# Kernel tuning notes

Measured on AMD Instinct MI355X. Metric: run time of the kernel, lower is better.

The kernel has to match this reference:

```python
import jax, jax.numpy as jnp
import numpy as np

HEADS = 16
DIM = 1024


def setup_inputs() -> dict:
    key = jax.random.key(0)
    ks = jax.random.split(key, 9)
    B, N, D = 2, 2048, DIM
    s = 1.0 / np.sqrt(D)
    x = jax.random.normal(ks[0], (B, N, D), dtype=jnp.float32)
    Wq = jax.random.normal(ks[1], (D, D), dtype=jnp.float32) * s
    Wk = jax.random.normal(ks[2], (D, D), dtype=jnp.float32) * s
    Wv = jax.random.normal(ks[3], (D, D), dtype=jnp.float32) * s
    Wo = jax.random.normal(ks[4], (D, D), dtype=jnp.float32) * s
    bq = jax.random.normal(ks[5], (D,), dtype=jnp.float32) * 0.01
    bk = jax.random.normal(ks[6], (D,), dtype=jnp.float32) * 0.01
    bv = jax.random.normal(ks[7], (D,), dtype=jnp.float32) * 0.01
    bo = jax.random.normal(ks[8], (D,), dtype=jnp.float32) * 0.01
    return {"x": x, "Wq": Wq, "bq": bq, "Wk": Wk, "bk": bk,
            "Wv": Wv, "bv": bv, "Wo": Wo, "bo": bo}


def reference(x, Wq, bq, Wk, bk, Wv, bv, Wo, bo):
    B, N, D = x.shape
    H = HEADS
    hd = D // H
    scale = hd ** (-0.5)
    # projections; split heads -> [B, H, N, hd]
    q = (x @ Wq + bq).reshape(B, N, H, hd).transpose(0, 2, 1, 3)
    k = (x @ Wk + bk).reshape(B, N, H, hd).transpose(0, 2, 1, 3)
    v = (x @ Wv + bv).reshape(B, N, H, hd).transpose(0, 2, 1, 3)
    # full [B, H, N, N] scores (faithful to naive torch implementation)
    attn = jnp.einsum('bhqd,bhkd->bhqk', q, k) * scale
    attn = jax.nn.softmax(attn, axis=-1)
    # dropout is identity in eval mode
    out = jnp.einsum('bhqk,bhkd->bhqd', attn, v)
    out = out.transpose(0, 2, 1, 3).reshape(B, N, D)
    return out @ Wo + bo
```

## Files before the change

kernel.cpp:

```cpp
#include <hip/hip_runtime.h>

#define HEADS 16
#define HD 64
#define SEQ 2048
#define DMODEL 1024
#define BATCH 2
#define MTOT (BATCH*SEQ)
#define KVB 64
#define NKH 16

typedef unsigned short u16;
typedef __bf16 bf16;
typedef bf16 bf16x8 __attribute__((ext_vector_type(8)));
typedef float f32x4 __attribute__((ext_vector_type(4)));
typedef float f32x16 __attribute__((ext_vector_type(16)));
typedef unsigned short u16x8 __attribute__((ext_vector_type(8)));
typedef unsigned short u16x4 __attribute__((ext_vector_type(4)));

static __device__ __forceinline__ u16 f2bf(float f) {
  bf16 b = (bf16)f;
  return __builtin_bit_cast(u16, b);
}

static __device__ __forceinline__ void async16(u16* lds_base, const u16* g) {
  __builtin_amdgcn_global_load_lds(
      (const __attribute__((address_space(1))) unsigned int*)g,
      (__attribute__((address_space(3))) unsigned int*)lds_base,
      16, 0, 0);
}

__global__ __launch_bounds__(256) void k_cvt(const float* __restrict__ in,
                                             u16* __restrict__ out, int n8) {
  int i = blockIdx.x * blockDim.x + threadIdx.x;
  if (i >= n8) return;
  const float4* p = (const float4*)(in + (size_t)i * 8);
  float4 a = p[0], b = p[1];
  u16x8 r;
  r[0] = f2bf(a.x); r[1] = f2bf(a.y); r[2] = f2bf(a.z); r[3] = f2bf(a.w);
  r[4] = f2bf(b.x); r[5] = f2bf(b.y); r[6] = f2bf(b.z); r[7] = f2bf(b.w);
  *(u16x8*)(out + (size_t)i * 8) = r;
}

__global__ __launch_bounds__(256) void k_cvtT(const float* __restrict__ W0, const float* __restrict__ W1,
                                              const float* __restrict__ W2, const float* __restrict__ W3,
                                              u16* __restrict__ T0, u16* __restrict__ T1,
                                              u16* __restrict__ T2, u16* __restrict__ T3) {
  const float* W = blockIdx.z == 0 ? W0 : blockIdx.z == 1 ? W1 : blockIdx.z == 2 ? W2 : W3;
  u16*         T = blockIdx.z == 0 ? T0 : blockIdx.z == 1 ? T1 : blockIdx.z == 2 ? T2 : T3;
  __shared__ u16 tile[64 * 68];
  int t = threadIdx.x;
  int kb = blockIdx.y * 64, nb = blockIdx.x * 64;
#pragma unroll
  for (int i = 0; i < 4; ++i) {
    int c = t * 4 + i;
    int row = c >> 4;
    int c4 = c & 15;
    float4 v = *(const float4*)&W[(size_t)(kb + row) * DMODEL + nb + c4 * 4];
    tile[row * 68 + c4 * 4 + 0] = f2bf(v.x);
    tile[row * 68 + c4 * 4 + 1] = f2bf(v.y);
    tile[row * 68 + c4 * 4 + 2] = f2bf(v.z);
    tile[row * 68 + c4 * 4 + 3] = f2bf(v.w);
  }
  __syncthreads();
#pragma unroll
  for (int i = 0; i < 2; ++i) {
    int c = t * 2 + i;
    int n = c >> 3;
    int k8 = c & 7;
    u16x8 v;
#pragma unroll
    for (int e = 0; e < 8; ++e) v[e] = tile[(k8 * 8 + e) * 68 + n];
    *(u16x8*)&T[(size_t)(nb + n) * DMODEL + kb + k8 * 8] = v;
  }
}

template <int MODE>
__global__ __launch_bounds__(256) void k_gemm(
    const u16* __restrict__ A,
    const u16* __restrict__ BT0, const u16* __restrict__ BT1, const u16* __restrict__ BT2,
    const float* __restrict__ b0, const float* __restrict__ b1, const float* __restrict__ b2,
    void* __restrict__ O0, void* __restrict__ O1, void* __restrict__ O2,
    int M, int N, int K) {
  const u16* BT = blockIdx.z == 0 ? BT0 : blockIdx.z == 1 ? BT1 : BT2;
  const float* bias = blockIdx.z == 0 ? b0 : blockIdx.z == 1 ? b1 : b2;
  void* Out = blockIdx.z == 0 ? O0 : blockIdx.z == 1 ? O1 : O2;

  __shared__ u16 Ads[128 * 32];
  __shared__ u16 Bds[128 * 32];
  int tid = threadIdx.x, wid = tid >> 6, lane = tid & 63;
  int r = lane & 15, g = lane >> 4;
  int wm = wid >> 1, wn = wid & 1;
  int m0 = blockIdx.y * 128, n0 = blockIdx.x * 128;

  f32x4 acc[4][4];
  f32x4 zero4 = {0.f, 0.f, 0.f, 0.f};
#pragma unroll
  for (int mt = 0; mt < 4; ++mt)
#pragma unroll
    for (int nt = 0; nt < 4; ++nt) acc[mt][nt] = zero4;

  int srow = lane >> 2;
  int scb = lane & 3;

  for (int k0 = 0; k0 < K; k0 += 32) {
#pragma unroll
    for (int tt = 0; tt < 2; ++tt) {
      int inst = wid * 2 + tt;
      int row = inst * 16 + srow;
      async16(&Ads[inst * 512], &A[(size_t)(m0 + row) * K + k0 + scb * 8]);
      async16(&Bds[inst * 512], &BT[(size_t)(n0 + row) * K + k0 + scb * 8]);
    }
    __syncthreads();
    bf16x8 af[4], bfv[4];
#pragma unroll
    for (int mt = 0; mt < 4; ++mt)
      af[mt] = *(const bf16x8*)&Ads[(wm * 64 + mt * 16 + r) * 32 + g * 8];
#pragma unroll
    for (int nt = 0; nt < 4; ++nt)
      bfv[nt] = *(const bf16x8*)&Bds[(wn * 64 + nt * 16 + r) * 32 + g * 8];
#pragma unroll
    for (int mt = 0; mt < 4; ++mt)
#pragma unroll
      for (int nt = 0; nt < 4; ++nt)
        acc[mt][nt] = __builtin_amdgcn_mfma_f32_16x16x32_bf16(af[mt], bfv[nt], acc[mt][nt], 0, 0, 0);
    __syncthreads();
  }

  const float qs = 0.18033688011112042f;
#pragma unroll
  for (int nt = 0; nt < 4; ++nt) {
    int col = n0 + wn * 64 + nt * 16 + r;
    float bv = bias[col];
#pragma unroll
    for (int mt = 0; mt < 4; ++mt) {
      int rowb = m0 + wm * 64 + mt * 16 + g * 4;
      if (MODE == 0) {
        int b = rowb >> 11;
        int h = col >> 6, d = col & (HD - 1);
        if (blockIdx.z == 2) {
          int n = rowb & (SEQ - 1);
          int np = (n & ~12) | ((n & 4) << 1) | ((n & 8) >> 1);
          u16x4 pk;
#pragma unroll
          for (int j = 0; j < 4; ++j) pk[j] = f2bf(acc[mt][nt][j] + bv);
          *(u16x4*)&((u16*)Out)[((size_t)((b * HEADS + h) * HD + d)) * SEQ + np] = pk;
        } else {
          float sc = (blockIdx.z == 0) ? qs : 1.0f;
#pragma unroll
          for (int j = 0; j < 4; ++j) {
            int row = rowb + j;
            int n = row & (SEQ - 1);
            ((u16*)Out)[((size_t)(b * HEADS + h) * SEQ + n) * HD + d] = f2bf((acc[mt][nt][j] + bv) * sc);
          }
        }
      } else {
#pragma unroll
        for (int j = 0; j < 4; ++j)
          ((float*)Out)[(size_t)(rowb + j) * N + col] = acc[mt][nt][j] + bv;
      }
    }
  }
}

__global__ __launch_bounds__(512, 4) void k_attn(const u16* __restrict__ Q,
                                                 const u16* __restrict__ Kg,
                                                 const u16* __restrict__ Vt,
                                                 u16* __restrict__ Oa) {
  __shared__ u16 lds[2][2][2][KVB * 64];

  int tid = threadIdx.x, wid = tid >> 6, lane = tid & 63;
  int l31 = lane & 31, hi = lane >> 5;
  int h = wid >> 2, s = wid & 3;

  int fid = blockIdx.y * gridDim.x + blockIdx.x;
  int swz = (fid & 7) * 64 + (fid >> 3);
  int qt = swz & 15;
  int bh = swz >> 4;

  const size_t kbase = (size_t)bh * SEQ * HD;
  const size_t vbase = (size_t)bh * HD * SEQ;
  int q0 = qt * 128 + s * 32;

  bf16x8 qf[4];
#pragma unroll
  for (int db = 0; db < 4; ++db)
    qf[db] = *(const bf16x8*)&Q[kbase + (size_t)(q0 + l31) * HD + db * 16 + hi * 8];

  int swz7 = l31 & 7;
  int coff[4];
#pragma unroll
  for (int i = 0; i < 4; ++i) coff[i] = ((2 * i + hi) ^ swz7) * 8;

  f32x16 zero16 = {0.f,0.f,0.f,0.f,0.f,0.f,0.f,0.f,0.f,0.f,0.f,0.f,0.f,0.f,0.f,0.f};
  f32x16 oacc0 = zero16, oacc1 = zero16, lacc = zero16;

  u16x8 onesb;
#pragma unroll
  for (int e = 0; e < 8; ++e) onesb[e] = 0x3F80;
  bf16x8 ones = __builtin_bit_cast(bf16x8, onesb);

  auto STAGE = [&](int b, int kc) {
    int kof = (h * NKH + kc) * KVB;
#pragma unroll
    for (int i = 0; i < 2; ++i) {
      int inst = s * 2 + i;
      int rr = inst * 8 + (lane >> 3);
      int ch = (lane & 7) ^ (rr & 7);
      async16(&lds[b][h][0][inst * 512], &Kg[kbase + (size_t)(kof + rr) * HD + ch * 8]);
      async16(&lds[b][h][1][inst * 512], &Vt[vbase + (size_t)rr * SEQ + kof + ch * 8]);
    }
  };

  auto BODY = [&](int buf, int kc) {
    if (kc + 1 < NKH) STAGE(buf ^ 1, kc + 1);

    const u16* Kb = &lds[buf][h][0][0];
    const u16* Vb = &lds[buf][h][1][0];

    f32x16 s0 = zero16, s1 = zero16;
#pragma unroll
    for (int db = 0; db < 4; ++db) {
      bf16x8 kf0 = *(const bf16x8*)&Kb[l31 * 64 + coff[db]];
      bf16x8 kf1 = *(const bf16x8*)&Kb[2048 + l31 * 64 + coff[db]];
      s0 = __builtin_amdgcn_mfma_f32_32x32x16_bf16(kf0, qf[db], s0, 0, 0, 0);
      s1 = __builtin_amdgcn_mfma_f32_32x32x16_bf16(kf1, qf[db], s1, 0, 0, 0);
    }

#pragma unroll
    for (int t = 0; t < 4; ++t) {
      u16x8 pk8;
#pragma unroll
      for (int e = 0; e < 8; ++e) {
        float sv = (t & 2) ? ((t & 1) ? s1[8 + e] : s1[e])
                           : ((t & 1) ? s0[8 + e] : s0[e]);
        pk8[e] = f2bf(__builtin_amdgcn_exp2f(sv));
      }
      bf16x8 pa = __builtin_bit_cast(bf16x8, pk8);

      lacc = __builtin_amdgcn_mfma_f32_32x32x16_bf16(pa, ones, lacc, 0, 0, 0);
      bf16x8 vf0 = *(const bf16x8*)&Vb[l31 * 64 + coff[t]];
      bf16x8 vf1 = *(const bf16x8*)&Vb[2048 + l31 * 64 + coff[t]];
      oacc0 = __builtin_amdgcn_mfma_f32_32x32x16_bf16(pa, vf0, oacc0, 0, 0, 0);
      oacc1 = __builtin_amdgcn_mfma_f32_32x32x16_bf16(pa, vf1, oacc1, 0, 0, 0);
    }

    asm volatile("s_waitcnt vmcnt(0)" ::: "memory");
    __builtin_amdgcn_sched_barrier(0);
    __builtin_amdgcn_s_barrier();
    __builtin_amdgcn_sched_barrier(0);
  };

  STAGE(0, 0);
  asm volatile("s_waitcnt vmcnt(0)" ::: "memory");
  __builtin_amdgcn_sched_barrier(0);
  __builtin_amdgcn_s_barrier();
  __builtin_amdgcn_sched_barrier(0);

  for (int kc = 0; kc < NKH; kc += 2) {
    BODY(0, kc);
    BODY(1, kc + 1);
  }

  float* cf = (float*)&lds[0][0][0][0];
  if (h == 1) {
#pragma unroll
    for (int r = 0; r < 16; ++r) {
      cf[s * 3072 + r * 64 + lane] = oacc0[r];
      cf[s * 3072 + 1024 + r * 64 + lane] = oacc1[r];
      cf[s * 3072 + 2048 + r * 64 + lane] = lacc[r];
    }
  }
  __syncthreads();
  if (h == 0) {
#pragma unroll
    for (int r = 0; r < 16; ++r) {
      oacc0[r] += cf[s * 3072 + r * 64 + lane];
      oacc1[r] += cf[s * 3072 + 1024 + r * 64 + lane];
      lacc[r]  += cf[s * 3072 + 2048 + r * 64 + lane];
    }
    int b = bh >> 4, hh = bh & 15;
#pragma unroll
    for (int reg = 0; reg < 16; ++reg) {
      int q = q0 + (reg & 3) + 8 * (reg >> 2) + 4 * hi;
      float inv = 1.0f / lacc[reg];
      size_t rowoff = ((size_t)(b * SEQ + q)) * DMODEL + hh * HD;
      Oa[rowoff + l31]      = f2bf(oacc0[reg] * inv);
      Oa[rowoff + 32 + l31] = f2bf(oacc1[reg] * inv);
    }
  }
}

extern "C" void kernel_launch(void* const* d_in, const int* in_sizes, int n_in,
                              void* d_out, int out_size, void* d_ws, size_t ws_size,
                              hipStream_t stream) {
  const float* x  = (const float*)d_in[0];
  const float* Wq = (const float*)d_in[1];
  const float* bq = (const float*)d_in[2];
  const float* Wk = (const float*)d_in[3];
  const float* bk = (const float*)d_in[4];
  const float* Wv = (const float*)d_in[5];
  const float* bv = (const float*)d_in[6];
  const float* Wo = (const float*)d_in[7];
  const float* bo = (const float*)d_in[8];

  char* ws = (char*)d_ws;
  const size_t MB = 1024 * 1024;
  u16* xb    = (u16*)(ws);
  u16* wqT   = (u16*)(ws + 8 * MB);
  u16* wkT   = (u16*)(ws + 10 * MB);
  u16* wvT   = (u16*)(ws + 12 * MB);
  u16* woT   = (u16*)(ws + 14 * MB);
  u16* qbuf  = (u16*)(ws + 16 * MB);
  u16* kbuf  = (u16*)(ws + 24 * MB);
  u16* vbufT = (u16*)(ws + 32 * MB);
  u16* abuf  = (u16*)(ws + 40 * MB);

  k_cvt<<<2048, 256, 0, stream>>>(x, xb, (MTOT * DMODEL) / 8);
  k_cvtT<<<dim3(16, 16, 4), 256, 0, stream>>>(Wq, Wk, Wv, Wo, wqT, wkT, wvT, woT);
  k_gemm<0><<<dim3(DMODEL / 128, MTOT / 128, 3), 256, 0, stream>>>(
      xb, wqT, wkT, wvT, bq, bk, bv, qbuf, kbuf, vbufT, MTOT, DMODEL, DMODEL);
  k_attn<<<dim3(SEQ / 128, BATCH * HEADS), 512, 0, stream>>>(qbuf, kbuf, vbufT, abuf);
  k_gemm<1><<<dim3(DMODEL / 128, MTOT / 128, 1), 256, 0, stream>>>(
      abuf, woT, woT, woT, bo, bo, bo, d_out, d_out, d_out, MTOT, DMODEL, DMODEL);
}
```

Measured before the change: 119.7 us.

## Double-buffer GEMM LDS tiles and raise wave priority around attention MFMAs

The projection GEMM now keeps two LDS buffers for the A and B tiles and issues the async loads for the next K-slice before computing on the current one. This overlaps global-to-LDS traffic with MFMA work and needs one barrier per step instead of two. The attention kernel wraps its MFMA groups in s_setprio so waves issuing matrix ops get scheduling priority over waves doing exp/pack work. The trade-offs are double the GEMM LDS footprint, which may lower occupancy, and the loop assumes K is a multiple of 64.

```diff
diff --git a/kernel.cpp b/kernel.cpp
--- a/kernel.cpp
+++ b/kernel.cpp
@@ -85,8 +85,8 @@
   const float* bias = blockIdx.z == 0 ? b0 : blockIdx.z == 1 ? b1 : b2;
   void* Out = blockIdx.z == 0 ? O0 : blockIdx.z == 1 ? O1 : O2;
 
-  __shared__ u16 Ads[128 * 32];
-  __shared__ u16 Bds[128 * 32];
+  __shared__ u16 Ads[2][128 * 32];
+  __shared__ u16 Bds[2][128 * 32];
   int tid = threadIdx.x, wid = tid >> 6, lane = tid & 63;
   int r = lane & 15, g = lane >> 4;
   int wm = wid >> 1, wn = wid & 1;
@@ -102,28 +102,45 @@
   int srow = lane >> 2;
   int scb = lane & 3;
 
-  for (int k0 = 0; k0 < K; k0 += 32) {
+  auto STAGE = [&](int b, int k0) {
 #pragma unroll
     for (int tt = 0; tt < 2; ++tt) {
       int inst = wid * 2 + tt;
       int row = inst * 16 + srow;
-      async16(&Ads[inst * 512], &A[(size_t)(m0 + row) * K + k0 + scb * 8]);
-      async16(&Bds[inst * 512], &BT[(size_t)(n0 + row) * K + k0 + scb * 8]);
-    }
-    __syncthreads();
+      async16(&Ads[b][inst * 512], &A[(size_t)(m0 + row) * K + k0 + scb * 8]);
+      async16(&Bds[b][inst * 512], &BT[(size_t)(n0 + row) * K + k0 + scb * 8]);
+    }
+  };
+
+  auto BODY = [&](int buf, int k0) {
+    if (k0 + 32 < K) STAGE(buf ^ 1, k0 + 32);
     bf16x8 af[4], bfv[4];
 #pragma unroll
     for (int mt = 0; mt < 4; ++mt)
-      af[mt] = *(const bf16x8*)&Ads[(wm * 64 + mt * 16 + r) * 32 + g * 8];
+      af[mt] = *(const bf16x8*)&Ads[buf][(wm * 64 + mt * 16 + r) * 32 + g * 8];
 #pragma unroll
     for (int nt = 0; nt < 4; ++nt)
-      bfv[nt] = *(const bf16x8*)&Bds[(wn * 64 + nt * 16 + r) * 32 + g * 8];
+      bfv[nt] = *(const bf16x8*)&Bds[buf][(wn * 64 + nt * 16 + r) * 32 + g * 8];
 #pragma unroll
     for (int mt = 0; mt < 4; ++mt)
 #pragma unroll
       for (int nt = 0; nt < 4; ++nt)
         acc[mt][nt] = __builtin_amdgcn_mfma_f32_16x16x32_bf16(af[mt], bfv[nt], acc[mt][nt], 0, 0, 0);
-    __syncthreads();
+    asm volatile("s_waitcnt vmcnt(0)" ::: "memory");
+    __builtin_amdgcn_sched_barrier(0);
+    __builtin_amdgcn_s_barrier();
+    __builtin_amdgcn_sched_barrier(0);
+  };
+
+  STAGE(0, 0);
+  asm volatile("s_waitcnt vmcnt(0)" ::: "memory");
+  __builtin_amdgcn_sched_barrier(0);
+  __builtin_amdgcn_s_barrier();
+  __builtin_amdgcn_sched_barrier(0);
+
+  for (int k0 = 0; k0 < K; k0 += 64) {
+    BODY(0, k0);
+    BODY(1, k0 + 32);
   }
 
   const float qs = 0.18033688011112042f;
@@ -218,6 +235,7 @@
     const u16* Vb = &lds[buf][h][1][0];
 
     f32x16 s0 = zero16, s1 = zero16;
+    __builtin_amdgcn_s_setprio(1);
 #pragma unroll
     for (int db = 0; db < 4; ++db) {
       bf16x8 kf0 = *(const bf16x8*)&Kb[l31 * 64 + coff[db]];
@@ -225,6 +243,7 @@
       s0 = __builtin_amdgcn_mfma_f32_32x32x16_bf16(kf0, qf[db], s0, 0, 0, 0);
       s1 = __builtin_amdgcn_mfma_f32_32x32x16_bf16(kf1, qf[db], s1, 0, 0, 0);
     }
+    __builtin_amdgcn_s_setprio(0);
 
 #pragma unroll
     for (int t = 0; t < 4; ++t) {
@@ -237,11 +256,13 @@
       }
       bf16x8 pa = __builtin_bit_cast(bf16x8, pk8);
 
-      lacc = __builtin_amdgcn_mfma_f32_32x32x16_bf16(pa, ones, lacc, 0, 0, 0);
       bf16x8 vf0 = *(const bf16x8*)&Vb[l31 * 64 + coff[t]];
       bf16x8 vf1 = *(const bf16x8*)&Vb[2048 + l31 * 64 + coff[t]];
+      __builtin_amdgcn_s_setprio(1);
+      lacc  = __builtin_amdgcn_mfma_f32_32x32x16_bf16(pa, ones, lacc, 0, 0, 0);
       oacc0 = __builtin_amdgcn_mfma_f32_32x32x16_bf16(pa, vf0, oacc0, 0, 0, 0);
       oacc1 = __builtin_amdgcn_mfma_f32_32x32x16_bf16(pa, vf1, oacc1, 0, 0, 0);
+      __builtin_amdgcn_s_setprio(0);
     }
 
     asm volatile("s_waitcnt vmcnt(0)" ::: "memory");
```

Measured after the change: 118.7 us. About the same (-0.8%).
